# Optimization experiments

Measured on AMD Instinct MI355X. Metric: run time of the kernel, lower is better.

The kernel has to match this reference:

```python
import jax, jax.numpy as jnp
import numpy as np

N_CODES = 8192
CODE_DIM = 256


def setup_inputs() -> dict:
    key = jax.random.key(0)
    kx, ke = jax.random.split(key)
    x = jax.random.normal(kx, (16, 4096, CODE_DIM), dtype=jnp.float32)
    # nn.Embedding weight initialized uniform(-1/n, 1/n)
    emb = jax.random.uniform(ke, (N_CODES, CODE_DIM), dtype=jnp.float32,
                             minval=-1.0 / N_CODES, maxval=1.0 / N_CODES)
    return {"x": x, "emb": emb}


def reference(x, emb):
    B, T, D = x.shape
    flat = x.reshape(-1, D)                                   # [BT, D]
    # squared euclidean distance: ||f||^2 - 2 f.e^T + ||e||^2  -> [BT, N]
    dist = ((flat * flat).sum(axis=1, keepdims=True)
            - 2.0 * flat @ emb.T
            + (emb * emb).sum(axis=1))
    idx = jnp.argmin(dist, axis=1)                            # [BT] int
    quant = emb[idx].reshape(x.shape)                         # [B, T, D]
    # commitment-style loss: mse(stop_grad(quant), x)
    loss = jnp.mean(jnp.square(jax.lax.stop_gradient(quant) - x))
    # straight-through estimator
    y = x + jax.lax.stop_gradient(quant - x)
    return y, idx.reshape(B, T), loss
```

## Files before the change

### kernel.cpp

```cpp
#include <hip/hip_runtime.h>
#include <stdint.h>


#define NCODES 8192
#define DDIM   256
#define BT     65536

#define TM     128
#define TN     128
#define NSEG   256
#define F4S    17

#define CAPC   48
#define MARGIN 7e-4f
#define CHUNKS 64

typedef float  f32x4  __attribute__((ext_vector_type(4)));
typedef __bf16 bf16x8 __attribute__((ext_vector_type(8)));

#define GLDS16(g, l) __builtin_amdgcn_global_load_lds(                         \
    (const __attribute__((address_space(1))) void*)(g),                        \
    (__attribute__((address_space(3))) void*)(l), 16, 0, 0)
#define GLDS4(g, l) __builtin_amdgcn_global_load_lds(                          \
    (const __attribute__((address_space(1))) void*)(g),                        \
    (__attribute__((address_space(3))) void*)(l), 4, 0, 0)

__device__ __forceinline__ unsigned int fenc(float f) {
  unsigned int u = __float_as_uint(f);
  return (u & 0x80000000u) ? ~u : (u | 0x80000000u);
}
__device__ __forceinline__ float fdec(unsigned int u) {
  unsigned int v = (u & 0x80000000u) ? (u ^ 0x80000000u) : ~u;
  return __uint_as_float(v);
}

__device__ __forceinline__ float np_pairwise256_sq(const float4* __restrict__ row) {
#pragma clang fp contract(off)
  float half[2];
  #pragma unroll
  for (int h = 0; h < 2; h++) {
    float r0,r1,r2,r3,r4,r5,r6,r7;
    float4 q0 = row[h*32 + 0];
    float4 q1 = row[h*32 + 1];
    r0 = q0.x*q0.x; r1 = q0.y*q0.y; r2 = q0.z*q0.z; r3 = q0.w*q0.w;
    r4 = q1.x*q1.x; r5 = q1.y*q1.y; r6 = q1.z*q1.z; r7 = q1.w*q1.w;
    #pragma unroll
    for (int g = 1; g < 16; g++) {
      q0 = row[h*32 + g*2];
      q1 = row[h*32 + g*2 + 1];
      r0 += q0.x*q0.x; r1 += q0.y*q0.y; r2 += q0.z*q0.z; r3 += q0.w*q0.w;
      r4 += q1.x*q1.x; r5 += q1.y*q1.y; r6 += q1.z*q1.z; r7 += q1.w*q1.w;
    }
    half[h] = ((r0+r1) + (r2+r3)) + ((r4+r5) + (r6+r7));
  }
  return half[0] + half[1];
}

__device__ __forceinline__ float exact_score(const float* __restrict__ xr,
                                             const float4* __restrict__ er,
                                             float Ar, float Cv) {
#pragma clang fp contract(off)
  float b = 0.0f;
  #pragma unroll 8
  for (int q = 0; q < 64; ++q) {
    float4 ev = er[q];
    b = fmaf(xr[q * 4 + 0], ev.x, b);
    b = fmaf(xr[q * 4 + 1], ev.y, b);
    b = fmaf(xr[q * 4 + 2], ev.z, b);
    b = fmaf(xr[q * 4 + 3], ev.w, b);
  }
  const float t1 = fmaf(-2.0f, b, Ar);
  return t1 + Cv;
}

__global__ void vq_pre_a(const float* __restrict__ x, float* __restrict__ Astage) {
  const int t = blockIdx.x * 256 + threadIdx.x;
  Astage[t] = np_pairwise256_sq((const float4*)(x + (size_t)t * DDIM));
}

__global__ void vq_pre_c(const float* __restrict__ emb, float* __restrict__ Cws) {
  const int c = blockIdx.x * 256 + threadIdx.x;
  Cws[c] = np_pairwise256_sq((const float4*)(emb + (size_t)c * DDIM));
}

__global__ void vq_init(float* __restrict__ oloss) { *oloss = 0.0f; }

__global__ void vq_pre_e(const float* __restrict__ emb, uint4* __restrict__ ebf) {
  const int g   = blockIdx.x * 256 + threadIdx.x;
  const int c   = g >> 5;
  const int blk = g & 31;
  const float4* e4 = (const float4*)(emb + (size_t)c * DDIM);
  float4 f0 = e4[blk*2], f1 = e4[blk*2 + 1];
  union { unsigned short us[8]; uint4 v; } pk;
  pk.us[0] = __builtin_bit_cast(unsigned short, (__bf16)f0.x);
  pk.us[1] = __builtin_bit_cast(unsigned short, (__bf16)f0.y);
  pk.us[2] = __builtin_bit_cast(unsigned short, (__bf16)f0.z);
  pk.us[3] = __builtin_bit_cast(unsigned short, (__bf16)f0.w);
  pk.us[4] = __builtin_bit_cast(unsigned short, (__bf16)f1.x);
  pk.us[5] = __builtin_bit_cast(unsigned short, (__bf16)f1.y);
  pk.us[6] = __builtin_bit_cast(unsigned short, (__bf16)f1.z);
  pk.us[7] = __builtin_bit_cast(unsigned short, (__bf16)f1.w);
  ebf[(size_t)c * 32 + (blk ^ (c & 7))] = pk.v;
}

__device__ __forceinline__ void stage_chunk(const char* __restrict__ ebf,
                                            const float* __restrict__ Cws,
                                            int ch, char* ebuf_dst,
                                            float* cs_dst, int tid) {
  const char* src = ebf + (size_t)ch * 65536 + (size_t)tid * 16;
  char* dst = ebuf_dst + (size_t)tid * 16;
  #pragma unroll
  for (int i = 0; i < 8; ++i) GLDS16(src + i * 8192, dst + i * 8192);
  if (tid < 128)
    GLDS4((const char*)Cws + (size_t)ch * 512 + (size_t)tid * 4,
          (char*)cs_dst + (size_t)tid * 4);
}

__global__ __launch_bounds__(512, 2)
void vq_filter(const float* __restrict__ x, const char* __restrict__ ebf,
               const float* __restrict__ Cws, int* __restrict__ cntG,
               int* __restrict__ candG) {
  __shared__ __align__(16) char ebuf[2][65536];
  __shared__ float Cs[3][128];
  __shared__ unsigned int umin[256];
  __shared__ int cntL[256];

  const int tid  = threadIdx.x;
  const int lane = tid & 63;
  const int wid  = tid >> 6;
  const int wm   = wid >> 2;
  const int wn   = wid & 3;
  const int l15  = lane & 15;
  const int lhi  = lane >> 4;
  const int tok0 = blockIdx.x * 256;

  if (tid < 256) { umin[tid] = 0xFFFFFFFFu; cntL[tid] = 0; }

  stage_chunk(ebf, Cws, 0, ebuf[0], Cs[0], tid);

  const float4* x4 = (const float4*)x;
  bf16x8 xb[4][8];
  #pragma unroll
  for (int n = 0; n < 4; ++n) {
    const size_t trow = (size_t)(tok0 + wn * 64 + n * 16 + l15) * 64;
    #pragma unroll
    for (int kk = 0; kk < 8; ++kk) {
      float4 f0 = x4[trow + kk * 8 + lhi * 2];
      float4 f1 = x4[trow + kk * 8 + lhi * 2 + 1];
      bf16x8 v;
      v[0] = (__bf16)f0.x; v[1] = (__bf16)f0.y; v[2] = (__bf16)f0.z; v[3] = (__bf16)f0.w;
      v[4] = (__bf16)f1.x; v[5] = (__bf16)f1.y; v[6] = (__bf16)f1.z; v[7] = (__bf16)f1.w;
      xb[n][kk] = v;
    }
  }
  __syncthreads();

  const f32x4 zf = {0.f, 0.f, 0.f, 0.f};

  for (int c = 0; c < CHUNKS; ++c) {
    stage_chunk(ebf, Cws, (c + 1) & 63, ebuf[(c + 1) & 1], Cs[(c + 1) % 3], tid);

    const char* ecur = ebuf[c & 1];
    f32x4 acc[4][4];
    #pragma unroll
    for (int kk = 0; kk < 8; ++kk) {
      bf16x8 a[4];
      #pragma unroll
      for (int m = 0; m < 4; ++m) {
        const int row = wm * 64 + m * 16 + l15;
        const int blk = (kk * 4 + lhi) ^ (row & 7);
        a[m] = *(const bf16x8*)(ecur + row * 512 + blk * 16);
      }
      #pragma unroll
      for (int m = 0; m < 4; ++m)
        #pragma unroll
        for (int n = 0; n < 4; ++n)
          acc[m][n] = __builtin_amdgcn_mfma_f32_16x16x32_bf16(
              a[m], xb[n][kk], (kk == 0) ? zf : acc[m][n], 0, 0, 0);
    }

    const float* Csc = Cs[c % 3];
    float cvals[4][4];
    #pragma unroll
    for (int m = 0; m < 4; ++m)
      #pragma unroll
      for (int r = 0; r < 4; ++r)
        cvals[m][r] = Csc[wm * 64 + m * 16 + lhi * 4 + r];

    #pragma unroll
    for (int n = 0; n < 4; ++n) {
      float mn = 1e30f;
      #pragma unroll
      for (int m = 0; m < 4; ++m)
        #pragma unroll
        for (int r = 0; r < 4; ++r)
          mn = fminf(mn, fmaf(-2.0f, acc[m][n][r], cvals[m][r]));
      atomicMin(&umin[wn * 64 + n * 16 + l15], fenc(mn));
    }

    __syncthreads();

    #pragma unroll
    for (int n = 0; n < 4; ++n) {
      const int t = wn * 64 + n * 16 + l15;
      const float thr = fdec(umin[t]) + MARGIN;
      #pragma unroll
      for (int m = 0; m < 4; ++m)
        #pragma unroll
        for (int r = 0; r < 4; ++r) {
          float s = fmaf(-2.0f, acc[m][n][r], cvals[m][r]);
          if (s <= thr) {
            int code = c * 128 + wm * 64 + m * 16 + lhi * 4 + r;
            int pos = atomicAdd(&cntL[t], 1);
            if (pos < CAPC) candG[(size_t)(tok0 + t) * CAPC + pos] = code;
          }
        }
    }
  }

  __syncthreads();
  if (tid < 256) cntG[tok0 + tid] = cntL[tid];
}

__global__ __launch_bounds__(256, 2)
void vq_rescore(const float* __restrict__ x, const float* __restrict__ emb,
                const float* __restrict__ Cws, const int* __restrict__ cntG,
                const int* __restrict__ candG, float* __restrict__ y,
                float* __restrict__ oidx, float* __restrict__ oloss) {
  __shared__ float xs[64 * 257];
  __shared__ float As[64];
  __shared__ int   idx_sh[64];
  __shared__ float red[4];
  __shared__ float rbv[256];
  __shared__ int   rbi[256];
  __shared__ int   ovf_list[64];
  __shared__ int   n_ovf;

  const int tid  = threadIdx.x;
  const int tok0 = blockIdx.x * 64;
  const float4* x4g = (const float4*)x;
  const float4* e4g = (const float4*)emb;

  if (tid == 0) n_ovf = 0;
  #pragma unroll
  for (int i = 0; i < 16; ++i) {
    const int g = tid + 256 * i, row = g >> 6, c4 = g & 63;
    float4 v = x4g[(size_t)(tok0 + row) * 64 + c4];
    float* p = &xs[row * 257 + c4 * 4];
    p[0] = v.x; p[1] = v.y; p[2] = v.z; p[3] = v.w;
  }
  if (tid < 64) As[tid] = oidx[tok0 + tid];
  __syncthreads();

  const int t  = tid >> 2;
  const int j0 = tid & 3;
  const int gt = tok0 + t;
  const int cnt = cntG[gt];
  const float* xr = &xs[t * 257];
  const float  Ar = As[t];

  if (cnt <= CAPC) {
    float best = 1e30f; int bid = 0x7FFFFFFF;
    for (int j = j0; j < cnt; j += 4) {
      const int c = candG[(size_t)gt * CAPC + j];
      const float s = exact_score(xr, e4g + (size_t)c * 64, Ar, Cws[c]);
      if (s < best || (s == best && c < bid)) { best = s; bid = c; }
    }
    #pragma unroll
    for (int off = 1; off <= 2; off <<= 1) {
      float ob = __shfl_xor(best, off);
      int   oi = __shfl_xor(bid, off);
      if (ob < best || (ob == best && oi < bid)) { best = ob; bid = oi; }
    }
    if (j0 == 0) { idx_sh[t] = bid; oidx[gt] = (float)(bid + 1); }
  } else if (j0 == 0) {
    const int p = atomicAdd(&n_ovf, 1);
    ovf_list[p] = t;
  }
  __syncthreads();

  for (int o = 0; o < n_ovf; ++o) {
    const int tt  = ovf_list[o];
    const float* xrr = &xs[tt * 257];
    const float  At  = As[tt];
    float bv = 1e30f; int bi2 = 0x7FFFFFFF;
    for (int c = tid; c < NCODES; c += 256) {
      const float s = exact_score(xrr, e4g + (size_t)c * 64, At, Cws[c]);
      if (s < bv || (s == bv && c < bi2)) { bv = s; bi2 = c; }
    }
    rbv[tid] = bv; rbi[tid] = bi2;
    __syncthreads();
    #pragma unroll
    for (int sft = 128; sft; sft >>= 1) {
      if (tid < sft) {
        const float v2 = rbv[tid + sft]; const int i2 = rbi[tid + sft];
        if (v2 < rbv[tid] || (v2 == rbv[tid] && i2 < rbi[tid])) {
          rbv[tid] = v2; rbi[tid] = i2;
        }
      }
      __syncthreads();
    }
    if (tid == 0) { idx_sh[tt] = rbi[0]; oidx[tok0 + tt] = (float)(rbi[0] + 1); }
    __syncthreads();
  }
  __syncthreads();

  float lsum = 0.0f;
  float4* y4 = (float4*)y;
  #pragma unroll
  for (int r = 0; r < 16; ++r) {
    const int g = tid + 256 * r, row = g >> 6, c4 = g & 63;
    const float4 ev = e4g[(size_t)idx_sh[row] * 64 + c4];
    const float4 xv = x4g[(size_t)(tok0 + row) * 64 + c4];
    y4[(size_t)(tok0 + row) * 64 + c4] = ev;
    const float dx = ev.x - xv.x, dy = ev.y - xv.y, dz = ev.z - xv.z, dw = ev.w - xv.w;
    lsum += dx * dx + dy * dy + dz * dz + dw * dw;
  }
  #pragma unroll
  for (int off = 32; off; off >>= 1) lsum += __shfl_down(lsum, off);
  if ((tid & 63) == 0) red[tid >> 6] = lsum;
  __syncthreads();
  if (tid == 0) atomicAdd(oloss, red[0] + red[1] + red[2] + red[3]);
}

__global__ void vq_fin(float* __restrict__ oloss) {
  *oloss = *oloss * (1.0f / 16777216.0f);
}

__global__ __launch_bounds__(256, 2)
void vq_main(const float* __restrict__ x, const float* __restrict__ emb,
             const float* __restrict__ Cws, float* __restrict__ y,
             float* __restrict__ oidx, float* __restrict__ oloss) {
  __shared__ float4 xs4[TM * F4S];
  __shared__ float4 es4[TN * F4S];
  __shared__ float  Cs[TN];
  __shared__ int    idx_sh[TM];
  __shared__ float  red[4];

  const int tid = threadIdx.x;
  const int ry = tid >> 4;
  const int rx = tid & 15;
  const int tok0 = blockIdx.x * TM;

  const float4* x4g = (const float4*)x;
  const float4* e4g = (const float4*)emb;

  float A_reg[8];
  #pragma unroll
  for (int m = 0; m < 8; m++) A_reg[m] = oidx[tok0 + ry + 16 * m];

  float best[8];
  int   i1[8];
  #pragma unroll
  for (int m = 0; m < 8; m++) { best[m] = 1e30f; i1[m] = 0; }

  float acc[8][8];

  for (int seg = 0; seg < NSEG; ++seg) {
    const int chunk = seg >> 2;
    const int kq = seg & 3;
    __syncthreads();
    #pragma unroll
    for (int h = 0; h < 2; h++) {
      float4 t[4];
      #pragma unroll
      for (int q = 0; q < 4; q++) {
        const int r = h * 4 + q;
        t[q] = x4g[(size_t)(tok0 + ry + 16 * r) * 64 + kq * 16 + rx];
      }
      #pragma unroll
      for (int q = 0; q < 4; q++) {
        const int r = h * 4 + q;
        xs4[(ry + 16 * r) * F4S + rx] = t[q];
      }
    }
    #pragma unroll
    for (int h = 0; h < 2; h++) {
      float4 t[4];
      #pragma unroll
      for (int q = 0; q < 4; q++) {
        const int r = h * 4 + q;
        t[q] = e4g[(size_t)(chunk * TN + ry + 16 * r) * 64 + kq * 16 + rx];
      }
      #pragma unroll
      for (int q = 0; q < 4; q++) {
        const int r = h * 4 + q;
        es4[(ry + 16 * r) * F4S + rx] = t[q];
      }
    }
    if (kq == 0 && tid < TN) Cs[tid] = Cws[chunk * TN + tid];
    __syncthreads();

    if (kq == 0) {
      #pragma unroll
      for (int m = 0; m < 8; m++)
        #pragma unroll
        for (int n = 0; n < 8; n++) acc[m][n] = 0.0f;
    }

    #pragma unroll
    for (int k4 = 0; k4 < 16; k4++) {
      float4 a[8], b[8];
      #pragma unroll
      for (int m = 0; m < 8; m++) a[m] = xs4[(ry + 16 * m) * F4S + k4];
      #pragma unroll
      for (int n = 0; n < 8; n++) b[n] = es4[(rx + 16 * n) * F4S + k4];
      #pragma unroll
      for (int m = 0; m < 8; m++)
        #pragma unroll
        for (int n = 0; n < 8; n++) {
          acc[m][n] = fmaf(a[m].x, b[n].x, acc[m][n]);
          acc[m][n] = fmaf(a[m].y, b[n].y, acc[m][n]);
          acc[m][n] = fmaf(a[m].z, b[n].z, acc[m][n]);
          acc[m][n] = fmaf(a[m].w, b[n].w, acc[m][n]);
        }
    }

    if (kq == 3) {
      const int c0 = chunk * TN;
      #pragma unroll
      for (int n = 0; n < 8; n++) {
        const float Cv = Cs[rx + 16 * n];
        const int c = c0 + rx + 16 * n;
        #pragma unroll
        for (int m = 0; m < 8; m++) {
          const float t1 = fmaf(-2.0f, acc[m][n], A_reg[m]);
          const float t2 = t1 + Cv;
          if (t2 < best[m]) { best[m] = t2; i1[m] = c; }
        }
      }
    }
  }

  __syncthreads();
  float* bv1 = (float*)xs4;
  int*   bi  = (int*)es4;
  #pragma unroll
  for (int m = 0; m < 8; m++) {
    bv1[(ry + 16 * m) * 16 + rx] = best[m];
    bi [(ry + 16 * m) * 16 + rx] = i1[m];
  }
  __syncthreads();
  if (tid < TM) {
    float v = bv1[tid * 16];
    int   id = bi[tid * 16];
    for (int t = 1; t < 16; t++) {
      const float vv = bv1[tid * 16 + t];
      const int   ii = bi [tid * 16 + t];
      if (vv < v || (vv == v && ii < id)) { v = vv; id = ii; }
    }
    idx_sh[tid] = id;
    oidx[tok0 + tid] = (float)(id + 1);
  }
  __syncthreads();

  float lsum = 0.0f;
  float4* y4 = (float4*)y;
  #pragma unroll
  for (int r = 0; r < 32; r++) {
    const int g = tid + 256 * r, row = g >> 6, c4 = g & 63;
    const float4 ev = e4g[(size_t)idx_sh[row] * 64 + c4];
    const float4 xv = x4g[(size_t)(tok0 + row) * 64 + c4];
    y4[(size_t)(tok0 + row) * 64 + c4] = ev;
    const float dx = ev.x - xv.x, dy = ev.y - xv.y, dz = ev.z - xv.z, dw = ev.w - xv.w;
    lsum += dx * dx + dy * dy + dz * dz + dw * dw;
  }
  #pragma unroll
  for (int off = 32; off; off >>= 1) lsum += __shfl_down(lsum, off);
  if ((tid & 63) == 0) red[tid >> 6] = lsum;
  __syncthreads();
  if (tid == 0) atomicAdd(oloss, red[0] + red[1] + red[2] + red[3]);
}

extern "C" void kernel_launch(void* const* d_in, const int* in_sizes, int n_in,
                              void* d_out, int out_size, void* d_ws, size_t ws_size,
                              hipStream_t stream) {
  const float* x   = (const float*)d_in[0];
  const float* emb = (const float*)d_in[1];

  float* y     = (float*)d_out;
  float* oidx  = y + (size_t)BT * DDIM;
  float* oloss = oidx + BT;

  char*  wsB   = (char*)d_ws;
  float* Cws   = (float*)wsB;
  int*   cntG  = (int*)(wsB + 32768);
  char*  ebf   = wsB + 32768 + 262144;
  int*   candG = (int*)(wsB + 294912 + 4194304);
  const size_t NEED = 294912 + 4194304 + (size_t)BT * CAPC * 4;

  vq_init <<<1, 1,           0, stream>>>(oloss);
  vq_pre_a<<<BT / 256, 256,  0, stream>>>(x, oidx);
  vq_pre_c<<<NCODES/256,256, 0, stream>>>(emb, Cws);

  if (ws_size >= NEED) {
    vq_pre_e  <<<1024, 256, 0, stream>>>(emb, (uint4*)ebf);
    vq_filter <<<256,  512, 0, stream>>>(x, ebf, Cws, cntG, candG);
    vq_rescore<<<1024, 256, 0, stream>>>(x, emb, Cws, cntG, candG, y, oidx, oloss);
  } else {
    vq_main   <<<BT / TM, 256, 0, stream>>>(x, emb, Cws, y, oidx, oloss);
  }
  vq_fin  <<<1, 1,           0, stream>>>(oloss);
}
```

Measured before the change: 811.0 us.

## Pack approximate scores into candidates, drop filter barrier, prune rescore candidates

The filter loop no longer waits at a mid-chunk barrier between the min update and the candidate pass. Each thread keeps a running per-token minimum, reduces it across lanes with shuffles, and issues only one atomicMin per token. Each candidate entry now packs a quantized approximate score above the code index, so the rescore kernel can find the best approximate key and skip exact fp32 dot products for candidates far beyond it. The overflow full scan scores two codes per iteration to add ILP. The risks are that the per-thread threshold may let more candidates overflow, and that the key quantization plus margin must still keep the true argmin.

```diff
diff --git a/kernel.cpp b/kernel.cpp
--- a/kernel.cpp
+++ b/kernel.cpp
@@ -14,6 +14,9 @@
 #define CAPC   48
 #define MARGIN 7e-4f
 #define CHUNKS 64
+#define KSCALE 1048576.0f
+#define KOFF   131072.0f
+#define KMARG  737
 
 typedef float  f32x4  __attribute__((ext_vector_type(4)));
 typedef __bf16 bf16x8 __attribute__((ext_vector_type(8)));
@@ -71,6 +74,27 @@
   }
   const float t1 = fmaf(-2.0f, b, Ar);
   return t1 + Cv;
+}
+
+__device__ __forceinline__ void exact_score2(const float* __restrict__ xr,
+                                             const float4* __restrict__ e1,
+                                             const float4* __restrict__ e2,
+                                             float Ar, float Cv1, float Cv2,
+                                             float& s1, float& s2) {
+#pragma clang fp contract(off)
+  float b1 = 0.0f, b2 = 0.0f;
+  #pragma unroll 8
+  for (int q = 0; q < 64; ++q) {
+    const float4 v1 = e1[q], v2 = e2[q];
+    const float x0 = xr[q * 4 + 0], x1 = xr[q * 4 + 1];
+    const float x2 = xr[q * 4 + 2], x3 = xr[q * 4 + 3];
+    b1 = fmaf(x0, v1.x, b1); b2 = fmaf(x0, v2.x, b2);
+    b1 = fmaf(x1, v1.y, b1); b2 = fmaf(x1, v2.y, b2);
+    b1 = fmaf(x2, v1.z, b1); b2 = fmaf(x2, v2.z, b2);
+    b1 = fmaf(x3, v1.w, b1); b2 = fmaf(x3, v2.w, b2);
+  }
+  s1 = fmaf(-2.0f, b1, Ar) + Cv1;
+  s2 = fmaf(-2.0f, b2, Ar) + Cv2;
 }
 
 __global__ void vq_pre_a(const float* __restrict__ x, float* __restrict__ Astage) {
@@ -121,7 +145,7 @@
                const float* __restrict__ Cws, int* __restrict__ cntG,
                int* __restrict__ candG) {
   __shared__ __align__(16) char ebuf[2][65536];
-  __shared__ float Cs[3][128];
+  __shared__ float Cs[2][128];
   __shared__ unsigned int umin[256];
   __shared__ int cntL[256];
 
@@ -156,9 +180,10 @@
   __syncthreads();
 
   const f32x4 zf = {0.f, 0.f, 0.f, 0.f};
+  float rmin[4] = {1e30f, 1e30f, 1e30f, 1e30f};
 
   for (int c = 0; c < CHUNKS; ++c) {
-    stage_chunk(ebf, Cws, (c + 1) & 63, ebuf[(c + 1) & 1], Cs[(c + 1) % 3], tid);
+    stage_chunk(ebf, Cws, (c + 1) & 63, ebuf[(c + 1) & 1], Cs[(c + 1) & 1], tid);
 
     const char* ecur = ebuf[c & 1];
     f32x4 acc[4][4];
@@ -179,7 +204,7 @@
               a[m], xb[n][kk], (kk == 0) ? zf : acc[m][n], 0, 0, 0);
     }
 
-    const float* Csc = Cs[c % 3];
+    const float* Csc = Cs[c & 1];
     float cvals[4][4];
     #pragma unroll
     for (int m = 0; m < 4; ++m)
@@ -189,36 +214,41 @@
 
     #pragma unroll
     for (int n = 0; n < 4; ++n) {
+      const int t = wn * 64 + n * 16 + l15;
+      float s[16];
       float mn = 1e30f;
-      #pragma unroll
-      for (int m = 0; m < 4; ++m)
-        #pragma unroll
-        for (int r = 0; r < 4; ++r)
-          mn = fminf(mn, fmaf(-2.0f, acc[m][n][r], cvals[m][r]));
-      atomicMin(&umin[wn * 64 + n * 16 + l15], fenc(mn));
-    }
-
-    __syncthreads();
-
-    #pragma unroll
-    for (int n = 0; n < 4; ++n) {
-      const int t = wn * 64 + n * 16 + l15;
-      const float thr = fdec(umin[t]) + MARGIN;
       #pragma unroll
       for (int m = 0; m < 4; ++m)
         #pragma unroll
         for (int r = 0; r < 4; ++r) {
-          float s = fmaf(-2.0f, acc[m][n][r], cvals[m][r]);
-          if (s <= thr) {
-            int code = c * 128 + wm * 64 + m * 16 + lhi * 4 + r;
-            int pos = atomicAdd(&cntL[t], 1);
-            if (pos < CAPC) candG[(size_t)(tok0 + t) * CAPC + pos] = code;
+          const float v = fmaf(-2.0f, acc[m][n][r], cvals[m][r]);
+          s[m * 4 + r] = v;
+          mn = fminf(mn, v);
+        }
+      mn = fminf(mn, __shfl_xor(mn, 16));
+      mn = fminf(mn, __shfl_xor(mn, 32));
+      if (mn < rmin[n]) {
+        rmin[n] = mn;
+        if (lhi == 0) atomicMin(&umin[t], fenc(mn));
+      }
+      const float thr = fminf(rmin[n], fdec(umin[t])) + MARGIN;
+      #pragma unroll
+      for (int m = 0; m < 4; ++m)
+        #pragma unroll
+        for (int r = 0; r < 4; ++r) {
+          if (s[m * 4 + r] <= thr) {
+            const int code = c * 128 + wm * 64 + m * 16 + lhi * 4 + r;
+            const int key  = (int)fmaf(s[m * 4 + r], KSCALE, KOFF);
+            const int pos  = atomicAdd(&cntL[t], 1);
+            if (pos < CAPC)
+              candG[(size_t)(tok0 + t) * CAPC + pos] = (key << 13) | code;
           }
         }
     }
-  }
-
-  __syncthreads();
+
+    __syncthreads();
+  }
+
   if (tid < 256) cntG[tok0 + tid] = cntL[tid];
 }
 
@@ -260,16 +290,24 @@
   const float  Ar = As[t];
 
   if (cnt <= CAPC) {
+    int pmin = 0x7FFFFFFF;
+    for (int j = j0; j < cnt; j += 4) pmin = min(pmin, candG[(size_t)gt * CAPC + j]);
+    pmin = min(pmin, __shfl_xor(pmin, 1));
+    pmin = min(pmin, __shfl_xor(pmin, 2));
+    const int thrk = (pmin >> 13) + KMARG;
     float best = 1e30f; int bid = 0x7FFFFFFF;
     for (int j = j0; j < cnt; j += 4) {
-      const int c = candG[(size_t)gt * CAPC + j];
-      const float s = exact_score(xr, e4g + (size_t)c * 64, Ar, Cws[c]);
-      if (s < best || (s == best && c < bid)) { best = s; bid = c; }
+      const int e = candG[(size_t)gt * CAPC + j];
+      if ((e >> 13) <= thrk) {
+        const int c = e & 8191;
+        const float s = exact_score(xr, e4g + (size_t)c * 64, Ar, Cws[c]);
+        if (s < best || (s == best && c < bid)) { best = s; bid = c; }
+      }
     }
     #pragma unroll
     for (int off = 1; off <= 2; off <<= 1) {
-      float ob = __shfl_xor(best, off);
-      int   oi = __shfl_xor(bid, off);
+      const float ob = __shfl_xor(best, off);
+      const int   oi = __shfl_xor(bid, off);
       if (ob < best || (ob == best && oi < bid)) { best = ob; bid = oi; }
     }
     if (j0 == 0) { idx_sh[t] = bid; oidx[gt] = (float)(bid + 1); }
@@ -284,9 +322,13 @@
     const float* xrr = &xs[tt * 257];
     const float  At  = As[tt];
     float bv = 1e30f; int bi2 = 0x7FFFFFFF;
-    for (int c = tid; c < NCODES; c += 256) {
-      const float s = exact_score(xrr, e4g + (size_t)c * 64, At, Cws[c]);
-      if (s < bv || (s == bv && c < bi2)) { bv = s; bi2 = c; }
+    for (int c0 = tid; c0 < NCODES; c0 += 512) {
+      const int c1 = c0 + 256;
+      float s1, s2;
+      exact_score2(xrr, e4g + (size_t)c0 * 64, e4g + (size_t)c1 * 64,
+                   At, Cws[c0], Cws[c1], s1, s2);
+      if (s1 < bv || (s1 == bv && c0 < bi2)) { bv = s1; bi2 = c0; }
+      if (s2 < bv || (s2 == bv && c1 < bi2)) { bv = s2; bi2 = c1; }
     }
     rbv[tid] = bv; rbi[tid] = bi2;
     __syncthreads();
```

After: 864.3 us. 6.6% more time.
